# Kernel tuning notes

Measured on AMD Instinct MI355X. Metric: run time of the kernel, lower is better.

The kernel has to match this reference:

```python
import jax, jax.numpy as jnp
import numpy as np

N_DYADIC = 0  # dyadic refinement order n (init kwarg)


def _solve_pde(inc):
    """Solve the signature-kernel Goursat PDE by finite differences.

    inc: (A, Mi, Ni) inner products <dx_i, dy_j> on the (refined) grid.
    Recurrence on grid K of shape (Mi+1, Ni+1):
      K[0,:] = K[:,0] = 1
      K[i,j] = K[i,j-1] + K[i-1,j] + K[i-1,j-1] * (inc[i-1,j-1] - 1)
    Implemented as an anti-diagonal wavefront (vectorized over batch and
    along each diagonal) so there is no O(M*N) sequential loop.
    Returns K[:, -1, -1], shape (A,).
    """
    A, Mi, Ni = inc.shape
    P = Mi + 1                      # number of grid rows
    ivec = jnp.arange(P)            # row index along a diagonal
    n_diags = Mi + Ni + 1           # diagonals d = i + j in [0, Mi+Ni]

    def step(carry, d):
        prev, prev2 = carry         # diagonals d-1 and d-2, shape (A, P)
        j = d - ivec                # column index for each row on diag d
        inc_d = inc[:, jnp.clip(ivec - 1, 0, Mi - 1),
                       jnp.clip(j - 1, 0, Ni - 1)]          # (A, P)
        # K[i,j-1] = prev[i]; K[i-1,j] = prev[i-1]; K[i-1,j-1] = prev2[i-1]
        interior = prev + jnp.roll(prev, 1, axis=1) \
                 + jnp.roll(prev2, 1, axis=1) * (inc_d - 1.0)
        in_grid = (j >= 0) & (j <= Ni)
        boundary = (ivec == 0) | (j == 0)
        new = jnp.where(in_grid, jnp.where(boundary, 1.0, interior), 0.0)
        return (new, prev), None

    init = (jnp.zeros((A, P), inc.dtype), jnp.zeros((A, P), inc.dtype))
    (last, _), _ = jax.lax.scan(step, init, jnp.arange(n_diags))
    return last[:, Mi]              # K at grid point (Mi, Ni)


def _sig_kernel(X, Y, n):
    """k(x_a, y_a) for each pair in the batch, via PDE solve."""
    f = 2 ** n
    dX = X[:, 1:] - X[:, :-1]                          # (A, M-1, D)
    dY = Y[:, 1:] - Y[:, :-1]                          # (A, N-1, D)
    C = jnp.einsum('amd,and->amn', dX, dY)             # (A, M-1, N-1)
    # dyadic refinement: each coarse increment split into 2^n equal pieces
    inc = jnp.repeat(jnp.repeat(C, f, axis=1), f, axis=2) / float(f * f)
    return _solve_pde(inc)


def setup_inputs() -> dict:
    key = jax.random.key(0)
    kx, ky = jax.random.split(key)
    A, M, D = 128, 512, 16
    # small-increment random walks so the signature kernel stays bounded
    X = 0.05 * jnp.cumsum(jax.random.normal(kx, (A, M, D), dtype=jnp.float32), axis=1)
    Y = 0.05 * jnp.cumsum(jax.random.normal(ky, (A, M, D), dtype=jnp.float32), axis=1)
    return {"X": X, "Y": Y}


def reference(X, Y):
    # SigLoss: mean_a [ k(x,x) + k(y,y) - 2 k(x,y) ]
    k_xx = _sig_kernel(X, X, N_DYADIC)
    k_yy = _sig_kernel(Y, Y, N_DYADIC)
    k_xy = _sig_kernel(X, Y, N_DYADIC)
    return jnp.mean(k_xx + k_yy - 2.0 * k_xy)
```

## Files before the change

### kernel.cpp

```cpp
#include <hip/hip_runtime.h>

#define D 16

typedef short bf16x8 __attribute__((ext_vector_type(8)));
typedef float f32x16 __attribute__((ext_vector_type(16)));
typedef float v2f __attribute__((ext_vector_type(2)));

template<int CTRL, int RMASK, bool BC>
__device__ __forceinline__ float dpp_add(float x) {
    int t = __builtin_amdgcn_update_dpp(0, __float_as_int(x), CTRL, RMASK, 0xF, BC);
    return x + __int_as_float(t);
}
__device__ __forceinline__ float wave_iscan(float x) {
    x = dpp_add<0x111, 0xF, true >(x);
    x = dpp_add<0x112, 0xF, true >(x);
    x = dpp_add<0x114, 0xF, true >(x);
    x = dpp_add<0x118, 0xF, true >(x);
    x = dpp_add<0x142, 0xA, false>(x);
    x = dpp_add<0x143, 0xC, false>(x);
    return x;
}

__device__ __forceinline__ short f2bf(float f) {
    unsigned u = __float_as_uint(f);
    unsigned r = u + 0x7FFFu + ((u >> 16) & 1u);
    return (short)(r >> 16);
}

__global__ __launch_bounds__(64, 1)
void sig_pde_kernel(const float* __restrict__ X, const float* __restrict__ Y,
                    float* __restrict__ out) {
    __shared__ float sinc[32 * 512];

    const int idx  = blockIdx.x;
    const int pair = idx >> 7;
    const int a    = idx & 127;
    const float* Pp = (pair == 1) ? Y : X;
    const float* Qp = (pair == 0) ? X : Y;
    const float* prow = Pp + (size_t)a * 512 * D;
    const float* qrow = Qp + (size_t)a * 512 * D;

    const int l  = threadIdx.x;
    const int lm = l & 31;
    const int kh = l >> 5;
    const int d0 = kh * 8;
    const bool lane0 = (l == 0);

    bf16x8 Bf[16];
    #pragma unroll
    for (int n = 0; n < 16; ++n) {
        int jj = 32 * n + lm - 1;
        if (jj < 0) jj = 0;
        const float4* y1 = (const float4*)(qrow + (size_t)(jj + 1) * D + d0);
        const float4* y0 = (const float4*)(qrow + (size_t)jj * D + d0);
        float4 h1 = y1[0], h0 = y0[0], g1 = y1[1], g0 = y0[1];
        bf16x8 f;
        f[0] = f2bf(h1.x - h0.x); f[1] = f2bf(h1.y - h0.y);
        f[2] = f2bf(h1.z - h0.z); f[3] = f2bf(h1.w - h0.w);
        f[4] = f2bf(g1.x - g0.x); f[5] = f2bf(g1.y - g0.y);
        f[6] = f2bf(g1.z - g0.z); f[7] = f2bf(g1.w - g0.w);
        Bf[n] = f;
    }

    auto loadA = [&](int b) -> bf16x8 {
        int ii = 32 * b + lm - 1;
        if (ii < 0) ii = 0;
        const float4* x1 = (const float4*)(prow + (size_t)(ii + 1) * D + d0);
        const float4* x0 = (const float4*)(prow + (size_t)ii * D + d0);
        float4 h1 = x1[0], h0 = x0[0], g1 = x1[1], g0 = x0[1];
        bf16x8 f;
        f[0] = f2bf(h1.x - h0.x); f[1] = f2bf(h1.y - h0.y);
        f[2] = f2bf(h1.z - h0.z); f[3] = f2bf(h1.w - h0.w);
        f[4] = f2bf(g1.x - g0.x); f[5] = f2bf(g1.y - g0.y);
        f[6] = f2bf(g1.z - g0.z); f[7] = f2bf(g1.w - g0.w);
        return f;
    };

    const int rot = (l >> 2) & 7;
    float* wbase = sinc + kh * 2048;

    unsigned eaddr[8];
    #pragma unroll
    for (int m = 0; m < 8; ++m)
        eaddr[m] = (unsigned)(size_t)((const char*)sinc
                                      + (8 * l + ((m + rot) & 7)) * 4);

    float s[8];
    #pragma unroll
    for (int m = 0; m < 8; ++m) s[m] = 0.0f;
    float B = 1.0f;

    v2f ghA[8], ghB[8];
    float eA[8], eB[8];

    const f32x16 accC = {-1.f,-1.f,-1.f,-1.f,-1.f,-1.f,-1.f,-1.f,
                         -1.f,-1.f,-1.f,-1.f,-1.f,-1.f,-1.f,-1.f};

#define WAIT8() do {                                                          \
        asm volatile("s_waitcnt lgkmcnt(8)" ::: "memory");                    \
        __builtin_amdgcn_sched_barrier(0);                                    \
    } while (0)

#define PREFA(BUF, RR) do {                                                   \
        asm volatile("ds_read_b32 %0, %1 offset:%c2"                          \
                     : "=v"(BUF[0]) : "v"(eaddr[0]), "i"((RR) * 2048));       \
        asm volatile("ds_read_b32 %0, %1 offset:%c2"                          \
                     : "=v"(BUF[1]) : "v"(eaddr[1]), "i"((RR) * 2048));       \
        asm volatile("ds_read_b32 %0, %1 offset:%c2"                          \
                     : "=v"(BUF[2]) : "v"(eaddr[2]), "i"((RR) * 2048));       \
        asm volatile("ds_read_b32 %0, %1 offset:%c2"                          \
                     : "=v"(BUF[3]) : "v"(eaddr[3]), "i"((RR) * 2048));       \
        asm volatile("ds_read_b32 %0, %1 offset:%c2"                          \
                     : "=v"(BUF[4]) : "v"(eaddr[4]), "i"((RR) * 2048));       \
        asm volatile("ds_read_b32 %0, %1 offset:%c2"                          \
                     : "=v"(BUF[5]) : "v"(eaddr[5]), "i"((RR) * 2048));       \
        asm volatile("ds_read_b32 %0, %1 offset:%c2"                          \
                     : "=v"(BUF[6]) : "v"(eaddr[6]), "i"((RR) * 2048));       \
        asm volatile("ds_read_b32 %0, %1 offset:%c2"                          \
                     : "=v"(BUF[7]) : "v"(eaddr[7]), "i"((RR) * 2048));       \
    } while (0)

#define GHBUILD(GH, E) do {                                                   \
        float p0_ = E[0] + 1.0f;  p0_ = lane0 ? 0.0f : p0_;                   \
        float c0_ = lane0 ? 0.0f : s[0];                                      \
        GH[0][0] = p0_; GH[0][1] = c0_;                                       \
        _Pragma("unroll")                                                     \
        for (int m_ = 1; m_ < 8; ++m_) {                                      \
            v2f pc_;                                                          \
            pc_[0] = E[m_] + 1.0f;                                            \
            pc_[1] = fmaf(s[m_ - 1], E[m_], s[m_]);                          \
            GH[m_] = GH[m_ - 1] + pc_;                                        \
        }                                                                     \
    } while (0)

#define SFMA(GH) do {                                                         \
        _Pragma("unroll")                                                     \
        for (int m_ = 0; m_ < 8; ++m_)                                        \
            s[m_] = fmaf(B, GH[m_][0], GH[m_][1]);                            \
    } while (0)

#define STEP1(GHC, GHN, EFREE, EREADY, RP) do {                               \
        PREFA(EFREE, RP);                                                     \
        WAIT8();                                                              \
        SFMA(GHC);                                                            \
        float S_ = s[7];                                                      \
        float W_ = wave_iscan(S_);                                            \
        GHBUILD(GHN, EREADY);                                                 \
        B = 1.0f + (W_ - S_);                                                 \
    } while (0)

#define SCAN_BLOCK(FROM) do {                                                 \
        PREFA(eA, (FROM));                                                    \
        PREFA(eB, (FROM) + 1);                                                \
        WAIT8();                           \
        GHBUILD(ghA, eA);                                                     \
        _Pragma("unroll")                                                     \
        for (int r_ = (FROM); r_ <= 31; ++r_) {                               \
            const int rp_ = (r_ + 2 <= 31) ? r_ + 2 : 31;                     \
            if (((r_ - (FROM)) & 1) == 0) STEP1(ghA, ghB, eA, eB, rp_);       \
            else                          STEP1(ghB, ghA, eB, eA, rp_);       \
        }                                                                     \
    } while (0)

    bf16x8 Acur = loadA(0);

    for (int b = 0; b < 16; ++b) {
        #pragma unroll
        for (int n = 0; n < 16; ++n) {
            f32x16 acc = __builtin_amdgcn_mfma_f32_32x32x16_bf16(Acur, Bf[n], accC, 0, 0, 0);
            float* p = wbase + 32 * n + (lm & ~7) + (((l & 7) + n) & 7);
            #pragma unroll
            for (int r = 0; r < 16; ++r)
                p[(r & 3) * 512 + (r >> 2) * 4096] = acc[r];
        }
        if (b < 15) Acur = loadA(b + 1);

        if (b == 0) SCAN_BLOCK(1);
        else        SCAN_BLOCK(0);
    }

#undef SCAN_BLOCK
#undef STEP1
#undef SFMA
#undef GHBUILD
#undef PREFA
#undef WAIT8

    if (l == 63) out[idx] = B + s[7];
}

__global__ void sig_reduce_kernel(const float* __restrict__ ws,
                                  float* __restrict__ out) {
    const int a = threadIdx.x;
    float v = ws[a] + ws[128 + a] - 2.0f * ws[256 + a];
    #pragma unroll
    for (int off = 32; off >= 1; off >>= 1) v += __shfl_down(v, off, 64);
    __shared__ float partial[2];
    if ((a & 63) == 0) partial[a >> 6] = v;
    __syncthreads();
    if (a == 0) out[0] = (partial[0] + partial[1]) * (1.0f / 128.0f);
}

extern "C" void kernel_launch(void* const* d_in, const int* in_sizes, int n_in,
                              void* d_out, int out_size, void* d_ws, size_t ws_size,
                              hipStream_t stream) {
    const float* X = (const float*)d_in[0];
    const float* Y = (const float*)d_in[1];
    float* out = (float*)d_out;
    float* ws  = (float*)d_ws;

    sig_pde_kernel<<<dim3(384), dim3(64), 0, stream>>>(X, Y, ws);
    sig_reduce_kernel<<<dim3(1), dim3(128), 0, stream>>>(ws, out);
}
```

Before: 83.44 us.

## Double-buffer LDS increments and interleave MFMA generation with the scan

Result: slower. 104.6 us (+25.4%).

```diff
diff --git a/kernel.cpp b/kernel.cpp
--- a/kernel.cpp
+++ b/kernel.cpp
@@ -30,7 +30,7 @@
 __global__ __launch_bounds__(64, 1)
 void sig_pde_kernel(const float* __restrict__ X, const float* __restrict__ Y,
                     float* __restrict__ out) {
-    __shared__ float sinc[32 * 512];
+    __shared__ float sinc[2 * 16 * 512];
 
     const int idx  = blockIdx.x;
     const int pair = idx >> 7;
@@ -44,6 +44,7 @@
     const int lm = l & 31;
     const int kh = l >> 5;
     const int d0 = kh * 8;
+    const int l7 = l & 7;
     const bool lane0 = (l == 0);
 
     bf16x8 Bf[16];
@@ -77,19 +78,23 @@
     };
 
     const int rot = (l >> 2) & 7;
-    float* wbase = sinc + kh * 2048;
 
     unsigned eaddr[8];
     #pragma unroll
     for (int m = 0; m < 8; ++m)
         eaddr[m] = (unsigned)(size_t)((const char*)sinc
                                       + (8 * l + ((m + rot) & 7)) * 4);
+    unsigned wsw[8];
+    #pragma unroll
+    for (int k = 0; k < 8; ++k) wsw[k] = (unsigned)(((l7 + k) & 7) * 4);
+    unsigned wb0r = (unsigned)(size_t)((const char*)sinc
+                                       + kh * 8192 + (lm & ~7) * 4);
+    unsigned wb1r = wb0r + 32768;
 
     float s[8];
     #pragma unroll
     for (int m = 0; m < 8; ++m) s[m] = 0.0f;
     float B = 1.0f;
-
     v2f ghA[8], ghB[8];
     float eA[8], eB[8];
 
@@ -100,24 +105,40 @@
         asm volatile("s_waitcnt lgkmcnt(8)" ::: "memory");                    \
         __builtin_amdgcn_sched_barrier(0);                                    \
     } while (0)
-
-#define PREFA(BUF, RR) do {                                                   \
-        asm volatile("ds_read_b32 %0, %1 offset:%c2"                          \
-                     : "=v"(BUF[0]) : "v"(eaddr[0]), "i"((RR) * 2048));       \
-        asm volatile("ds_read_b32 %0, %1 offset:%c2"                          \
-                     : "=v"(BUF[1]) : "v"(eaddr[1]), "i"((RR) * 2048));       \
-        asm volatile("ds_read_b32 %0, %1 offset:%c2"                          \
-                     : "=v"(BUF[2]) : "v"(eaddr[2]), "i"((RR) * 2048));       \
-        asm volatile("ds_read_b32 %0, %1 offset:%c2"                          \
-                     : "=v"(BUF[3]) : "v"(eaddr[3]), "i"((RR) * 2048));       \
-        asm volatile("ds_read_b32 %0, %1 offset:%c2"                          \
-                     : "=v"(BUF[4]) : "v"(eaddr[4]), "i"((RR) * 2048));       \
-        asm volatile("ds_read_b32 %0, %1 offset:%c2"                          \
-                     : "=v"(BUF[5]) : "v"(eaddr[5]), "i"((RR) * 2048));       \
-        asm volatile("ds_read_b32 %0, %1 offset:%c2"                          \
-                     : "=v"(BUF[6]) : "v"(eaddr[6]), "i"((RR) * 2048));       \
-        asm volatile("ds_read_b32 %0, %1 offset:%c2"                          \
-                     : "=v"(BUF[7]) : "v"(eaddr[7]), "i"((RR) * 2048));       \
+#define WAIT0() do {                                                          \
+        asm volatile("s_waitcnt lgkmcnt(0)" ::: "memory");                    \
+        __builtin_amdgcn_sched_barrier(0);                                    \
+    } while (0)
+
+#define PREFA(BUF, BOFF) do {                                                 \
+        asm volatile("ds_read_b32 %0, %1 offset:%c2"                          \
+                     : "=v"(BUF[0]) : "v"(eaddr[0]), "i"(BOFF));              \
+        asm volatile("ds_read_b32 %0, %1 offset:%c2"                          \
+                     : "=v"(BUF[1]) : "v"(eaddr[1]), "i"(BOFF));              \
+        asm volatile("ds_read_b32 %0, %1 offset:%c2"                          \
+                     : "=v"(BUF[2]) : "v"(eaddr[2]), "i"(BOFF));              \
+        asm volatile("ds_read_b32 %0, %1 offset:%c2"                          \
+                     : "=v"(BUF[3]) : "v"(eaddr[3]), "i"(BOFF));              \
+        asm volatile("ds_read_b32 %0, %1 offset:%c2"                          \
+                     : "=v"(BUF[4]) : "v"(eaddr[4]), "i"(BOFF));              \
+        asm volatile("ds_read_b32 %0, %1 offset:%c2"                          \
+                     : "=v"(BUF[5]) : "v"(eaddr[5]), "i"(BOFF));              \
+        asm volatile("ds_read_b32 %0, %1 offset:%c2"                          \
+                     : "=v"(BUF[6]) : "v"(eaddr[6]), "i"(BOFF));              \
+        asm volatile("ds_read_b32 %0, %1 offset:%c2"                          \
+                     : "=v"(BUF[7]) : "v"(eaddr[7]), "i"(BOFF));              \
+    } while (0)
+
+#define WSLICE(ACC, HI, N, WBR) do {                                          \
+        unsigned wa_ = (WBR) + 128u * (N) + wsw[(N) & 7];                     \
+        asm volatile("ds_write_b32 %0, %1"              :: "v"(wa_), "v"(ACC[8*(HI)+0])); \
+        asm volatile("ds_write_b32 %0, %1 offset:2048"  :: "v"(wa_), "v"(ACC[8*(HI)+1])); \
+        asm volatile("ds_write_b32 %0, %1 offset:4096"  :: "v"(wa_), "v"(ACC[8*(HI)+2])); \
+        asm volatile("ds_write_b32 %0, %1 offset:6144"  :: "v"(wa_), "v"(ACC[8*(HI)+3])); \
+        asm volatile("ds_write_b32 %0, %1 offset:16384" :: "v"(wa_), "v"(ACC[8*(HI)+4])); \
+        asm volatile("ds_write_b32 %0, %1 offset:18432" :: "v"(wa_), "v"(ACC[8*(HI)+5])); \
+        asm volatile("ds_write_b32 %0, %1 offset:20480" :: "v"(wa_), "v"(ACC[8*(HI)+6])); \
+        asm volatile("ds_write_b32 %0, %1 offset:22528" :: "v"(wa_), "v"(ACC[8*(HI)+7])); \
     } while (0)
 
 #define GHBUILD(GH, E) do {                                                   \
@@ -139,51 +160,137 @@
             s[m_] = fmaf(B, GH[m_][0], GH[m_][1]);                            \
     } while (0)
 
-#define STEP1(GHC, GHN, EFREE, EREADY, RP) do {                               \
-        PREFA(EFREE, RP);                                                     \
+#define ROW0G(RB, DOG) do {                                                   \
+        PREFA(eA, (RB) + 2 * 2048);                                           \
         WAIT8();                                                              \
-        SFMA(GHC);                                                            \
-        float S_ = s[7];                                                      \
-        float W_ = wave_iscan(S_);                                            \
-        GHBUILD(GHN, EREADY);                                                 \
+        SFMA(ghA);                                                            \
+        float S_ = s[7]; float W_ = wave_iscan(S_);                           \
+        GHBUILD(ghB, eB);                                                     \
         B = 1.0f + (W_ - S_);                                                 \
-    } while (0)
-
-#define SCAN_BLOCK(FROM) do {                                                 \
-        PREFA(eA, (FROM));                                                    \
-        PREFA(eB, (FROM) + 1);                                                \
-        WAIT8();                           \
+        if (DOG) accg = __builtin_amdgcn_mfma_f32_32x32x16_bf16(Acur, Bf[0], accC, 0, 0, 0); \
+    } while (0)
+
+#define ROWSTD(R, RB, WBR, HI, DOG) do {                                      \
+        if ((R) & 1) { PREFA(eB, (RB) + ((R) + 2) * 2048); }                  \
+        else         { PREFA(eA, (RB) + ((R) + 2) * 2048); }                  \
+        WAIT8();                                                              \
+        if (DOG) WSLICE(accg, HI, (R) - 1, WBR);                              \
+        if ((R) & 1) {                                                        \
+            SFMA(ghB);                                                        \
+            float S_ = s[7]; float W_ = wave_iscan(S_);                       \
+            GHBUILD(ghA, eA);                                                 \
+            B = 1.0f + (W_ - S_);                                             \
+        } else {                                                              \
+            SFMA(ghA);                                                        \
+            float S_ = s[7]; float W_ = wave_iscan(S_);                       \
+            GHBUILD(ghB, eB);                                                 \
+            B = 1.0f + (W_ - S_);                                             \
+        }                                                                     \
+        if (DOG) accg = __builtin_amdgcn_mfma_f32_32x32x16_bf16(Acur, Bf[R], accC, 0, 0, 0); \
+    } while (0)
+
+#define ROW14G(WBR, HI, DOG) do {                                             \
+        if (DOG) { WAIT8(); WSLICE(accg, HI, 13, WBR); }                      \
+        else     { WAIT0(); }                                                 \
+        SFMA(ghA);                                                            \
+        float S_ = s[7]; float W_ = wave_iscan(S_);                           \
+        GHBUILD(ghB, eB);                                                     \
+        B = 1.0f + (W_ - S_);                                                 \
+        if (DOG) accg = __builtin_amdgcn_mfma_f32_32x32x16_bf16(Acur, Bf[14], accC, 0, 0, 0); \
+    } while (0)
+
+#define ROW15G(WBR, HI, NRB) do {                                             \
+        WSLICE(accg, HI, 14, WBR);                                            \
+        accg = __builtin_amdgcn_mfma_f32_32x32x16_bf16(Acur, Bf[15], accC, 0, 0, 0); \
+        WSLICE(accg, HI, 15, WBR);                                            \
+        PREFA(eA, (NRB) + 0);                                                 \
+        PREFA(eB, (NRB) + 2048);                                              \
+        WAIT8();                                                              \
+        SFMA(ghB);                                                            \
+        float S_ = s[7]; float W_ = wave_iscan(S_);                           \
         GHBUILD(ghA, eA);                                                     \
-        _Pragma("unroll")                                                     \
-        for (int r_ = (FROM); r_ <= 31; ++r_) {                               \
-            const int rp_ = (r_ + 2 <= 31) ? r_ + 2 : 31;                     \
-            if (((r_ - (FROM)) & 1) == 0) STEP1(ghA, ghB, eA, eB, rp_);       \
-            else                          STEP1(ghB, ghA, eB, eA, rp_);       \
-        }                                                                     \
+        B = 1.0f + (W_ - S_);                                                 \
+    } while (0)
+
+#define ROW15L() do {                                                         \
+        SFMA(ghB);                                                            \
+        float S_ = s[7]; float W_ = wave_iscan(S_);                           \
+        B = 1.0f + (W_ - S_);                                                 \
     } while (0)
 
     bf16x8 Acur = loadA(0);
-
-    for (int b = 0; b < 16; ++b) {
-        #pragma unroll
-        for (int n = 0; n < 16; ++n) {
-            f32x16 acc = __builtin_amdgcn_mfma_f32_32x32x16_bf16(Acur, Bf[n], accC, 0, 0, 0);
-            float* p = wbase + 32 * n + (lm & ~7) + (((l & 7) + n) & 7);
-            #pragma unroll
-            for (int r = 0; r < 16; ++r)
-                p[(r & 3) * 512 + (r >> 2) * 4096] = acc[r];
-        }
-        if (b < 15) Acur = loadA(b + 1);
-
-        if (b == 0) SCAN_BLOCK(1);
-        else        SCAN_BLOCK(0);
+    bf16x8 Anext = Acur;
+    f32x16 accg;
+
+    #pragma unroll
+    for (int n = 0; n < 16; ++n) {
+        f32x16 t = __builtin_amdgcn_mfma_f32_32x32x16_bf16(Acur, Bf[n], accC, 0, 0, 0);
+        WSLICE(t, 0, n, wb0r);
     }
-
-#undef SCAN_BLOCK
-#undef STEP1
+    accg = __builtin_amdgcn_mfma_f32_32x32x16_bf16(Acur, Bf[0], accC, 0, 0, 0);
+    PREFA(eB, 0 + 1 * 2048);
+    PREFA(eA, 0 + 2 * 2048);
+    WAIT8();
+    GHBUILD(ghB, eB);
+
+    ROWSTD( 1, 0, wb1r, 1, 1); ROWSTD( 2, 0, wb1r, 1, 1);
+    ROWSTD( 3, 0, wb1r, 1, 1);
+    Anext = loadA(1);
+    ROWSTD( 4, 0, wb1r, 1, 1); ROWSTD( 5, 0, wb1r, 1, 1);
+    ROWSTD( 6, 0, wb1r, 1, 1); ROWSTD( 7, 0, wb1r, 1, 1);
+    ROWSTD( 8, 0, wb1r, 1, 1); ROWSTD( 9, 0, wb1r, 1, 1);
+    ROWSTD(10, 0, wb1r, 1, 1); ROWSTD(11, 0, wb1r, 1, 1);
+    ROWSTD(12, 0, wb1r, 1, 1); ROWSTD(13, 0, wb1r, 1, 1);
+    ROW14G(wb1r, 1, 1);
+    ROW15G(wb1r, 1, 32768);
+    Acur = Anext;
+
+    for (int p = 0; p < 15; ++p) {
+        ROW0G(32768, 1);
+        ROWSTD( 1, 32768, wb0r, 0, 1); ROWSTD( 2, 32768, wb0r, 0, 1);
+        ROWSTD( 3, 32768, wb0r, 0, 1); ROWSTD( 4, 32768, wb0r, 0, 1);
+        ROWSTD( 5, 32768, wb0r, 0, 1); ROWSTD( 6, 32768, wb0r, 0, 1);
+        ROWSTD( 7, 32768, wb0r, 0, 1); ROWSTD( 8, 32768, wb0r, 0, 1);
+        ROWSTD( 9, 32768, wb0r, 0, 1); ROWSTD(10, 32768, wb0r, 0, 1);
+        ROWSTD(11, 32768, wb0r, 0, 1); ROWSTD(12, 32768, wb0r, 0, 1);
+        ROWSTD(13, 32768, wb0r, 0, 1);
+        ROW14G(wb0r, 0, 1);
+        ROW15G(wb0r, 0, 0);
+        ROW0G(0, 1);
+        ROWSTD( 1, 0, wb1r, 1, 1); ROWSTD( 2, 0, wb1r, 1, 1);
+        ROWSTD( 3, 0, wb1r, 1, 1);
+        if (p < 14) Anext = loadA(p + 2);
+        ROWSTD( 4, 0, wb1r, 1, 1); ROWSTD( 5, 0, wb1r, 1, 1);
+        ROWSTD( 6, 0, wb1r, 1, 1); ROWSTD( 7, 0, wb1r, 1, 1);
+        ROWSTD( 8, 0, wb1r, 1, 1); ROWSTD( 9, 0, wb1r, 1, 1);
+        ROWSTD(10, 0, wb1r, 1, 1); ROWSTD(11, 0, wb1r, 1, 1);
+        ROWSTD(12, 0, wb1r, 1, 1); ROWSTD(13, 0, wb1r, 1, 1);
+        ROW14G(wb1r, 1, 1);
+        ROW15G(wb1r, 1, 32768);
+        if (p < 14) Acur = Anext;
+    }
+
+    ROW0G(32768, 0);
+    ROWSTD( 1, 32768, wb0r, 0, 0); ROWSTD( 2, 32768, wb0r, 0, 0);
+    ROWSTD( 3, 32768, wb0r, 0, 0); ROWSTD( 4, 32768, wb0r, 0, 0);
+    ROWSTD( 5, 32768, wb0r, 0, 0); ROWSTD( 6, 32768, wb0r, 0, 0);
+    ROWSTD( 7, 32768, wb0r, 0, 0); ROWSTD( 8, 32768, wb0r, 0, 0);
+    ROWSTD( 9, 32768, wb0r, 0, 0); ROWSTD(10, 32768, wb0r, 0, 0);
+    ROWSTD(11, 32768, wb0r, 0, 0); ROWSTD(12, 32768, wb0r, 0, 0);
+    ROWSTD(13, 32768, wb0r, 0, 0);
+    ROW14G(wb0r, 0, 0);
+    ROW15L();
+
+#undef ROW15L
+#undef ROW15G
+#undef ROW14G
+#undef ROWSTD
+#undef ROW0G
 #undef SFMA
 #undef GHBUILD
+#undef WSLICE
 #undef PREFA
+#undef WAIT0
 #undef WAIT8
 
     if (l == 63) out[idx] = B + s[7];
```
